# Kernel optimization log

Hardware: AMD Instinct MI355X
Metric: run time of the kernel (lower is better)

## Reference

```python
import jax, jax.numpy as jnp
import numpy as np

DIM, DEPTH, HEADS, DIM_HEAD, MLP_DIM = 512, 6, 8, 64, 2048
INNER = HEADS * DIM_HEAD
EPS = 1e-5


def _layernorm(x, s, b):
    mu = jnp.mean(x, axis=-1, keepdims=True)
    var = jnp.mean(jnp.square(x - mu), axis=-1, keepdims=True)
    return (x - mu) * jax.lax.rsqrt(var + EPS) * s + b


def setup_inputs() -> dict:
    key = jax.random.key(0)
    ks = jax.random.split(key, 12)
    d = {
        "x": jax.random.normal(ks[0], (8, 1024, DIM), dtype=jnp.float32),
        "ln1_s": jnp.ones((DEPTH, DIM), jnp.float32),
        "ln1_b": jnp.zeros((DEPTH, DIM), jnp.float32),
        "w_qkv": jax.random.normal(ks[1], (DEPTH, DIM, 3 * INNER), dtype=jnp.float32) * (DIM ** -0.5),
        "w_out": jax.random.normal(ks[2], (DEPTH, INNER, DIM), dtype=jnp.float32) * (INNER ** -0.5),
        "b_out": jnp.zeros((DEPTH, DIM), jnp.float32),
        "ln2_s": jnp.ones((DEPTH, DIM), jnp.float32),
        "ln2_b": jnp.zeros((DEPTH, DIM), jnp.float32),
        "w1": jax.random.normal(ks[3], (DEPTH, DIM, MLP_DIM), dtype=jnp.float32) * (DIM ** -0.5),
        "b1": jnp.zeros((DEPTH, MLP_DIM), jnp.float32),
        "w2": jax.random.normal(ks[4], (DEPTH, MLP_DIM, DIM), dtype=jnp.float32) * (MLP_DIM ** -0.5),
        "b2": jnp.zeros((DEPTH, DIM), jnp.float32),
    }
    return d


def reference(x, ln1_s, ln1_b, w_qkv, w_out, b_out, ln2_s, ln2_b, w1, b1, w2, b2):
    b, n, _ = x.shape
    scale = DIM_HEAD ** -0.5
    for i in range(DEPTH):
        # --- PreNorm Attention with residual ---
        h = _layernorm(x, ln1_s[i], ln1_b[i])
        qkv = h @ w_qkv[i]                                  # [b, n, 3*inner]
        q, k, v = jnp.split(qkv, 3, axis=-1)
        q = q.reshape(b, n, HEADS, DIM_HEAD)
        k = k.reshape(b, n, HEADS, DIM_HEAD)
        v = v.reshape(b, n, HEADS, DIM_HEAD)
        dots = jnp.einsum('bihd,bjhd->bhij', q, k) * scale  # [b, h, n, n]
        attn = jax.nn.softmax(dots, axis=-1)
        out = jnp.einsum('bhij,bjhd->bihd', attn, v).reshape(b, n, INNER)
        x = out @ w_out[i] + b_out[i] + x
        # --- PreNorm FeedForward with residual ---
        h = _layernorm(x, ln2_s[i], ln2_b[i])
        h = jax.nn.gelu(h @ w1[i] + b1[i], approximate=False)
        x = h @ w2[i] + b2[i] + x
    return x
```

## Files before the change

kernel.cpp:

```cpp
#include <hip/hip_runtime.h>
#include <cstdint>
#include <cstddef>

#define M_TOK 8192
#define DIMM  512
#define HEADS 8
#define DH    64
#define MLPD  2048
#define DEPTH 6

typedef unsigned short u16;
typedef unsigned int   u32;
typedef __attribute__((ext_vector_type(8))) short short8;
typedef __attribute__((ext_vector_type(4))) float f32x4;

__device__ __forceinline__ float bf2f(u16 u){ return __uint_as_float(((u32)u) << 16); }
__device__ __forceinline__ u16 f2bf(float f){
    u32 x = __float_as_uint(f);
    u32 r = x + 0x7fffu + ((x >> 16) & 1u);
    return (u16)(r >> 16);
}

__global__ void k_transpose_cvt(const float* __restrict__ in, u16* __restrict__ out, int R, int C){
    __shared__ u16 tile[32][33];
    size_t zoff = (size_t)blockIdx.z * R * C;
    in += zoff; out += zoff;
    int c0 = blockIdx.x * 32, r0 = blockIdx.y * 32;
    int tx = threadIdx.x, ty = threadIdx.y;
    #pragma unroll
    for (int i = 0; i < 32; i += 8)
        tile[ty + i][tx] = f2bf(in[(size_t)(r0 + ty + i) * C + c0 + tx]);
    __syncthreads();
    #pragma unroll
    for (int i = 0; i < 32; i += 8)
        out[(size_t)(c0 + ty + i) * R + r0 + tx] = tile[tx][ty + i];
}

__global__ __launch_bounds__(64) void k_layernorm(const float* __restrict__ x,
                                                  const float* __restrict__ s,
                                                  const float* __restrict__ b,
                                                  u16* __restrict__ out){
    int row = blockIdx.x;
    int lane = threadIdx.x;
    const float* xp = x + (size_t)row * DIMM + lane * 8;
    float v[8];
    #pragma unroll
    for (int c = 0; c < 8; c++) v[c] = xp[c];
    float sum = 0.f, sq = 0.f;
    #pragma unroll
    for (int c = 0; c < 8; c++){ sum += v[c]; sq += v[c] * v[c]; }
    #pragma unroll
    for (int m = 32; m >= 1; m >>= 1){
        sum += __shfl_xor(sum, m);
        sq  += __shfl_xor(sq,  m);
    }
    float mu  = sum * (1.f / DIMM);
    float var = sq * (1.f / DIMM) - mu * mu;
    float rs  = rsqrtf(var + 1e-5f);
    u16* op = out + (size_t)row * DIMM + lane * 8;
    #pragma unroll
    for (int c = 0; c < 8; c++){
        int col = lane * 8 + c;
        op[c] = f2bf((v[c] - mu) * rs * s[col] + b[col]);
    }
}

__device__ __forceinline__ float gelu_exact(float v){
    return 0.5f * v * (1.f + erff(v * 0.70710678118654752f));
}

#define LDT64 72

template<int MODE>
__global__ __launch_bounds__(256) void k_gemm128b(const u16* __restrict__ A,
                                                  const u16* __restrict__ Bt,
                                                  const float* __restrict__ bias,
                                                  u16* __restrict__ Cout,
                                                  int M, int N, int K){
    __shared__ u16 As[128 * LDT64];
    __shared__ u16 Bs[128 * LDT64];
    int m0 = blockIdx.y * 128, n0 = blockIdx.x * 128;
    int t = threadIdx.x;
    int w = t >> 6, lane = t & 63;
    int mi = lane & 15, quad = lane >> 4;
    int wr = w >> 1, wc = w & 1;
    int srow = t >> 1, scol = (t & 1) * 32;

    const u16* ag = A  + (size_t)(m0 + srow) * K + scol;
    const u16* bg = Bt + (size_t)(n0 + srow) * K + scol;

    f32x4 acc[4][4];
    #pragma unroll
    for (int mt = 0; mt < 4; mt++)
        #pragma unroll
        for (int nt = 0; nt < 4; nt++) acc[mt][nt] = (f32x4){0.f, 0.f, 0.f, 0.f};

    for (int k0 = 0; k0 < K; k0 += 64){
        uint4 a0 = *(const uint4*)(ag + k0);
        uint4 a1 = *(const uint4*)(ag + k0 + 8);
        uint4 a2 = *(const uint4*)(ag + k0 + 16);
        uint4 a3 = *(const uint4*)(ag + k0 + 24);
        uint4 b0 = *(const uint4*)(bg + k0);
        uint4 b1 = *(const uint4*)(bg + k0 + 8);
        uint4 b2 = *(const uint4*)(bg + k0 + 16);
        uint4 b3 = *(const uint4*)(bg + k0 + 24);
        __syncthreads();
        *(uint4*)&As[srow * LDT64 + scol]      = a0;
        *(uint4*)&As[srow * LDT64 + scol + 8]  = a1;
        *(uint4*)&As[srow * LDT64 + scol + 16] = a2;
        *(uint4*)&As[srow * LDT64 + scol + 24] = a3;
        *(uint4*)&Bs[srow * LDT64 + scol]      = b0;
        *(uint4*)&Bs[srow * LDT64 + scol + 8]  = b1;
        *(uint4*)&Bs[srow * LDT64 + scol + 16] = b2;
        *(uint4*)&Bs[srow * LDT64 + scol + 24] = b3;
        __syncthreads();
        #pragma unroll
        for (int kk = 0; kk < 64; kk += 32){
            short8 af[4], bf[4];
            #pragma unroll
            for (int mt = 0; mt < 4; mt++)
                af[mt] = *(const short8*)&As[(wr * 64 + mt * 16 + mi) * LDT64 + kk + quad * 8];
            #pragma unroll
            for (int nt = 0; nt < 4; nt++)
                bf[nt] = *(const short8*)&Bs[(wc * 64 + nt * 16 + mi) * LDT64 + kk + quad * 8];
            #pragma unroll
            for (int mt = 0; mt < 4; mt++)
                #pragma unroll
                for (int nt = 0; nt < 4; nt++)
                    acc[mt][nt] = __builtin_amdgcn_mfma_f32_16x16x32_bf16(af[mt], bf[nt], acc[mt][nt], 0, 0, 0);
        }
    }

    float bv[4];
    if (MODE == 1){
        #pragma unroll
        for (int nt = 0; nt < 4; nt++) bv[nt] = bias[n0 + wc * 64 + nt * 16 + mi];
    }
    __syncthreads();
    u16* cs = &As[w * 16 * LDT64];
    int erow = lane >> 2, ecol = (lane & 3) * 16;
    #pragma unroll
    for (int mt = 0; mt < 4; mt++){
        #pragma unroll
        for (int nt = 0; nt < 4; nt++)
            #pragma unroll
            for (int r = 0; r < 4; r++){
                float v = acc[mt][nt][r];
                if (MODE == 1) v = gelu_exact(v + bv[nt]);
                cs[(quad * 4 + r) * LDT64 + nt * 16 + mi] = f2bf(v);
            }
        uint4 c0 = *(const uint4*)&cs[erow * LDT64 + ecol];
        uint4 c1 = *(const uint4*)&cs[erow * LDT64 + ecol + 8];
        u16* cp = Cout + (size_t)(m0 + wr * 64 + mt * 16 + erow) * N + n0 + wc * 64 + ecol;
        *(uint4*)cp       = c0;
        *(uint4*)(cp + 8) = c1;
    }
}

__global__ __launch_bounds__(256) void k_gemm64_res(const u16* __restrict__ A,
                                                    const u16* __restrict__ Bt,
                                                    const float* __restrict__ bias,
                                                    float* __restrict__ xres,
                                                    int M, int N, int K){
    __shared__ u16 As[64 * LDT64];
    __shared__ u16 Bs[64 * LDT64];
    int m0 = blockIdx.y * 64, n0 = blockIdx.x * 64;
    int t = threadIdx.x;
    int w = t >> 6, lane = t & 63;
    int mi = lane & 15, quad = lane >> 4;
    int srow = t >> 2, scol = (t & 3) * 16;

    const u16* ag = A  + (size_t)(m0 + srow) * K + scol;
    const u16* bg = Bt + (size_t)(n0 + srow) * K + scol;

    f32x4 acc[4];
    #pragma unroll
    for (int tt = 0; tt < 4; tt++) acc[tt] = (f32x4){0.f, 0.f, 0.f, 0.f};

    for (int k0 = 0; k0 < K; k0 += 64){
        uint4 a0 = *(const uint4*)(ag + k0);
        uint4 a1 = *(const uint4*)(ag + k0 + 8);
        uint4 b0 = *(const uint4*)(bg + k0);
        uint4 b1 = *(const uint4*)(bg + k0 + 8);
        __syncthreads();
        *(uint4*)&As[srow * LDT64 + scol]     = a0;
        *(uint4*)&As[srow * LDT64 + scol + 8] = a1;
        *(uint4*)&Bs[srow * LDT64 + scol]     = b0;
        *(uint4*)&Bs[srow * LDT64 + scol + 8] = b1;
        __syncthreads();
        short8 af0 = *(const short8*)&As[(w * 16 + mi) * LDT64 + quad * 8];
        short8 af1 = *(const short8*)&As[(w * 16 + mi) * LDT64 + quad * 8 + 32];
        #pragma unroll
        for (int tt = 0; tt < 4; tt++){
            short8 bf0 = *(const short8*)&Bs[(tt * 16 + mi) * LDT64 + quad * 8];
            short8 bf1 = *(const short8*)&Bs[(tt * 16 + mi) * LDT64 + quad * 8 + 32];
            acc[tt] = __builtin_amdgcn_mfma_f32_16x16x32_bf16(af0, bf0, acc[tt], 0, 0, 0);
            acc[tt] = __builtin_amdgcn_mfma_f32_16x16x32_bf16(af1, bf1, acc[tt], 0, 0, 0);
        }
    }

    float bv[4];
    #pragma unroll
    for (int tt = 0; tt < 4; tt++) bv[tt] = bias[n0 + tt * 16 + mi];
    __syncthreads();
    float* cs = (w < 2) ? ((float*)As + w * 16 * LDT64)
                        : ((float*)Bs + (w - 2) * 16 * LDT64);
    #pragma unroll
    for (int tt = 0; tt < 4; tt++)
        #pragma unroll
        for (int r = 0; r < 4; r++)
            cs[(quad * 4 + r) * LDT64 + tt * 16 + mi] = acc[tt][r] + bv[tt];
    int erow = lane >> 2, ecol = (lane & 3) * 16;
    float* xp = xres + (size_t)(m0 + w * 16 + erow) * N + n0 + ecol;
    #pragma unroll
    for (int j = 0; j < 4; j++){
        float4 cv = *(const float4*)&cs[erow * LDT64 + ecol + j * 4];
        float4 xv = *(const float4*)(xp + j * 4);
        xv.x += cv.x; xv.y += cv.y; xv.z += cv.z; xv.w += cv.w;
        *(float4*)(xp + j * 4) = xv;
    }
}

#define LDK 72
#define C1_LOG2E 0.18033688011112042f
#define C2_LOG2E 11.541560327111707f

__global__ __launch_bounds__(256) void k_flash(const u16* __restrict__ qkv, u16* __restrict__ out){
    __shared__ u16 Ks[64 * LDK];
    __shared__ u16 Vt[80 * LDK];
    __shared__ u16 Ps[4][32 * LDK];
    int qt = blockIdx.x, h = blockIdx.y, b = blockIdx.z;
    int t = threadIdx.x;
    int w = t >> 6, lane = t & 63;
    int mi = lane & 15, quad = lane >> 4;

    for (int i = t; i < 16 * 64; i += 256){
        int d = i >> 6, kk = i & 63;
        Vt[(64 + d) * LDK + kk] = 0x3F80;
    }

    const u16* base = qkv + ((size_t)b * 1024) * 1536;
    int hoff = h * 64;

    short8 qf[2][2];
    #pragma unroll
    for (int qh = 0; qh < 2; qh++){
        int qrow = qt * 128 + w * 32 + qh * 16 + mi;
        const u16* qp = base + (size_t)qrow * 1536 + hoff + quad * 8;
        qf[qh][0] = *(const short8*)(qp);
        qf[qh][1] = *(const short8*)(qp + 32);
    }

    f32x4 o[2][4];
    f32x4 lacc[2];
    #pragma unroll
    for (int qh = 0; qh < 2; qh++){
        #pragma unroll
        for (int nb = 0; nb < 4; nb++) o[qh][nb] = (f32x4){0.f, 0.f, 0.f, 0.f};
        lacc[qh] = (f32x4){0.f, 0.f, 0.f, 0.f};
    }

    int kkey = t >> 2, kseg = t & 3;
    const u16* kgp = base + (size_t)kkey * 1536 + 512 + hoff + kseg * 16;
    int vkey = lane, vdg = w;
    const u16* vgp = base + (size_t)vkey * 1536 + 1024 + hoff + vdg * 16;

    for (int kt = 0; kt < 16; kt++){
        size_t koff = (size_t)kt * 64 * 1536;
        uint4 kv0 = *(const uint4*)(kgp + koff);
        uint4 kv1 = *(const uint4*)(kgp + koff + 8);
        uint4 vv0 = *(const uint4*)(vgp + koff);
        uint4 vv1 = *(const uint4*)(vgp + koff + 8);
        __syncthreads();
        *(uint4*)&Ks[kkey * LDK + kseg * 16]     = kv0;
        *(uint4*)&Ks[kkey * LDK + kseg * 16 + 8] = kv1;
        u16 vtmp[16];
        *(uint4*)&vtmp[0] = vv0;
        *(uint4*)&vtmp[8] = vv1;
        #pragma unroll
        for (int i = 0; i < 16; i++)
            Vt[(vdg * 16 + i) * LDK + vkey] = vtmp[i];
        __syncthreads();

        short8 kb[4][2];
        #pragma unroll
        for (int nb = 0; nb < 4; nb++){
            kb[nb][0] = *(const short8*)&Ks[(nb * 16 + mi) * LDK + quad * 8];
            kb[nb][1] = *(const short8*)&Ks[(nb * 16 + mi) * LDK + quad * 8 + 32];
        }
        #pragma unroll
        for (int qh = 0; qh < 2; qh++){
            #pragma unroll
            for (int nb = 0; nb < 4; nb++){
                f32x4 z = (f32x4){0.f, 0.f, 0.f, 0.f};
                z = __builtin_amdgcn_mfma_f32_16x16x32_bf16(qf[qh][0], kb[nb][0], z, 0, 0, 0);
                z = __builtin_amdgcn_mfma_f32_16x16x32_bf16(qf[qh][1], kb[nb][1], z, 0, 0, 0);
                #pragma unroll
                for (int r = 0; r < 4; r++)
                    Ps[w][(qh * 16 + quad * 4 + r) * LDK + nb * 16 + mi] =
                        f2bf(exp2f(fmaf(z[r], C1_LOG2E, -C2_LOG2E)));
            }
        }
        short8 vb[4][2], lb[2];
        #pragma unroll
        for (int nb = 0; nb < 4; nb++){
            vb[nb][0] = *(const short8*)&Vt[(nb * 16 + mi) * LDK + quad * 8];
            vb[nb][1] = *(const short8*)&Vt[(nb * 16 + mi) * LDK + quad * 8 + 32];
        }
        lb[0] = *(const short8*)&Vt[(64 + mi) * LDK + quad * 8];
        lb[1] = *(const short8*)&Vt[(64 + mi) * LDK + quad * 8 + 32];
        #pragma unroll
        for (int qh = 0; qh < 2; qh++){
            const short8 a0 = *(const short8*)&Ps[w][(qh * 16 + mi) * LDK + quad * 8];
            const short8 a1 = *(const short8*)&Ps[w][(qh * 16 + mi) * LDK + quad * 8 + 32];
            #pragma unroll
            for (int nb = 0; nb < 4; nb++){
                o[qh][nb] = __builtin_amdgcn_mfma_f32_16x16x32_bf16(a0, vb[nb][0], o[qh][nb], 0, 0, 0);
                o[qh][nb] = __builtin_amdgcn_mfma_f32_16x16x32_bf16(a1, vb[nb][1], o[qh][nb], 0, 0, 0);
            }
            lacc[qh] = __builtin_amdgcn_mfma_f32_16x16x32_bf16(a0, lb[0], lacc[qh], 0, 0, 0);
            lacc[qh] = __builtin_amdgcn_mfma_f32_16x16x32_bf16(a1, lb[1], lacc[qh], 0, 0, 0);
        }
    }
    #pragma unroll
    for (int qh = 0; qh < 2; qh++){
        float invl[4];
        #pragma unroll
        for (int r = 0; r < 4; r++) invl[r] = 1.f / lacc[qh][r];
        u16* op = out + ((size_t)b * 1024 + qt * 128 + w * 32 + qh * 16) * 512 + hoff;
        #pragma unroll
        for (int nb = 0; nb < 4; nb++)
            #pragma unroll
            for (int r = 0; r < 4; r++)
                op[(quad * 4 + r) * 512 + nb * 16 + mi] = f2bf(o[qh][nb][r] * invl[r]);
    }
}

extern "C" void kernel_launch(void* const* d_in, const int* in_sizes, int n_in,
                              void* d_out, int out_size, void* d_ws, size_t ws_size,
                              hipStream_t stream){
    const float* x_in  = (const float*)d_in[0];
    const float* ln1_s = (const float*)d_in[1];
    const float* ln1_b = (const float*)d_in[2];
    const float* w_qkv = (const float*)d_in[3];
    const float* w_out = (const float*)d_in[4];
    const float* b_out = (const float*)d_in[5];
    const float* ln2_s = (const float*)d_in[6];
    const float* ln2_b = (const float*)d_in[7];
    const float* w1    = (const float*)d_in[8];
    const float* b1    = (const float*)d_in[9];
    const float* w2    = (const float*)d_in[10];
    const float* b2    = (const float*)d_in[11];
    float* out = (float*)d_out;

    char* ws = (char*)d_ws;
    float* x_f32 = (float*)ws;   ws += (size_t)M_TOK * DIMM * 4;
    u16* bufA    = (u16*)ws;     ws += (size_t)M_TOK * DIMM * 2;
    u16* bufB    = (u16*)ws;     ws += (size_t)M_TOK * MLPD * 2;
    u16* wbase   = (u16*)ws;
    size_t per_layer_w = (size_t)(1536 + 512 + 2048 + 2048) * 512;

    size_t used_big = (size_t)(ws - (char*)d_ws) + per_layer_w * 2 * DEPTH;
    bool big = (ws_size >= used_big);

    u16* ln_out   = bufA;
    u16* attn_out = bufA;
    u16* qkv      = bufB;
    u16* mlp_h    = bufB;

    size_t x_bytes = (size_t)M_TOK * DIMM * sizeof(float);
    hipMemcpyAsync(x_f32, x_in, x_bytes, hipMemcpyDeviceToDevice, stream);

    const size_t off_qkv = 0;
    const size_t off_out = (size_t)1536 * 512;
    const size_t off_w1  = off_out + (size_t)512 * 512;
    const size_t off_w2  = off_w1 + (size_t)2048 * 512;

    if (big){
        k_transpose_cvt<<<dim3(48, 16, 6), dim3(32, 8), 0, stream>>>(w_qkv, wbase + off_qkv * DEPTH, 512, 1536);
        k_transpose_cvt<<<dim3(16, 16, 6), dim3(32, 8), 0, stream>>>(w_out, wbase + off_out * DEPTH, 512, 512);
        k_transpose_cvt<<<dim3(64, 16, 6), dim3(32, 8), 0, stream>>>(w1,    wbase + off_w1  * DEPTH, 512, 2048);
        k_transpose_cvt<<<dim3(16, 64, 6), dim3(32, 8), 0, stream>>>(w2,    wbase + off_w2  * DEPTH, 2048, 512);
    }

    for (int i = 0; i < DEPTH; i++){
        u16 *wqkvT, *woutT, *w1T, *w2T;
        if (big){
            wqkvT = wbase + off_qkv * DEPTH + (size_t)i * 1536 * 512;
            woutT = wbase + off_out * DEPTH + (size_t)i * 512 * 512;
            w1T   = wbase + off_w1  * DEPTH + (size_t)i * 2048 * 512;
            w2T   = wbase + off_w2  * DEPTH + (size_t)i * 512 * 2048;
        } else {
            wqkvT = wbase + off_qkv; woutT = wbase + off_out;
            w1T   = wbase + off_w1;  w2T   = wbase + off_w2;
            k_transpose_cvt<<<dim3(48, 16), dim3(32, 8), 0, stream>>>(w_qkv + (size_t)i * 512 * 1536, wqkvT, 512, 1536);
            k_transpose_cvt<<<dim3(16, 16), dim3(32, 8), 0, stream>>>(w_out + (size_t)i * 512 * 512,  woutT, 512, 512);
            k_transpose_cvt<<<dim3(64, 16), dim3(32, 8), 0, stream>>>(w1    + (size_t)i * 512 * 2048, w1T,   512, 2048);
            k_transpose_cvt<<<dim3(16, 64), dim3(32, 8), 0, stream>>>(w2    + (size_t)i * 2048 * 512, w2T,   2048, 512);
        }

        k_layernorm<<<dim3(M_TOK), dim3(64), 0, stream>>>(x_f32, ln1_s + i * 512, ln1_b + i * 512, ln_out);
        k_gemm128b<0><<<dim3(12, 64), dim3(256), 0, stream>>>(ln_out, wqkvT, nullptr, qkv,
                                                              M_TOK, 1536, 512);
        k_flash<<<dim3(8, 8, 8), dim3(256), 0, stream>>>(qkv, attn_out);
        k_gemm64_res<<<dim3(8, 128), dim3(256), 0, stream>>>(attn_out, woutT, b_out + i * 512, x_f32,
                                                             M_TOK, 512, 512);
        k_layernorm<<<dim3(M_TOK), dim3(64), 0, stream>>>(x_f32, ln2_s + i * 512, ln2_b + i * 512, ln_out);
        k_gemm128b<1><<<dim3(16, 64), dim3(256), 0, stream>>>(ln_out, w1T, b1 + i * 2048, mlp_h,
                                                              M_TOK, 2048, 512);
        k_gemm64_res<<<dim3(8, 128), dim3(256), 0, stream>>>(mlp_h, w2T, b2 + i * 512, x_f32,
                                                             M_TOK, 512, 2048);
    }
    hipMemcpyAsync(out, x_f32, x_bytes, hipMemcpyDeviceToDevice, stream);
}
```

Before: 1.262 ms.

## Prefetch GEMM tiles into registers, swap grid order, truncate softmax bf16 conversion

Both GEMM kernels now load the next K-slab from global memory into registers before the current slab's MFMA work runs. The aim is to hide global load latency behind compute. All GEMM and flash launches swap grid axes so consecutive blocks walk along M (or along batch-head) instead of N, which changes L2 reuse of weight and activation tiles. The attention probability conversion to bf16 now truncates instead of rounding, which saves a few ALU ops per element at some cost in precision.

```diff
diff --git a/kernel.cpp b/kernel.cpp
--- a/kernel.cpp
+++ b/kernel.cpp
@@ -20,6 +20,7 @@
     u32 r = x + 0x7fffu + ((x >> 16) & 1u);
     return (u16)(r >> 16);
 }
+__device__ __forceinline__ u16 f2bf_t(float f){ return (u16)(__float_as_uint(f) >> 16); }
 
 __global__ void k_transpose_cvt(const float* __restrict__ in, u16* __restrict__ out, int R, int C){
     __shared__ u16 tile[32][33];
@@ -79,7 +80,7 @@
                                                   int M, int N, int K){
     __shared__ u16 As[128 * LDT64];
     __shared__ u16 Bs[128 * LDT64];
-    int m0 = blockIdx.y * 128, n0 = blockIdx.x * 128;
+    int m0 = blockIdx.x * 128, n0 = blockIdx.y * 128;
     int t = threadIdx.x;
     int w = t >> 6, lane = t & 63;
     int mi = lane & 15, quad = lane >> 4;
@@ -95,24 +96,26 @@
         #pragma unroll
         for (int nt = 0; nt < 4; nt++) acc[mt][nt] = (f32x4){0.f, 0.f, 0.f, 0.f};
 
+    uint4 pa[4], pb[4];
+    #pragma unroll
+    for (int j = 0; j < 4; j++){
+        pa[j] = *(const uint4*)(ag + j * 8);
+        pb[j] = *(const uint4*)(bg + j * 8);
+    }
+
     for (int k0 = 0; k0 < K; k0 += 64){
-        uint4 a0 = *(const uint4*)(ag + k0);
-        uint4 a1 = *(const uint4*)(ag + k0 + 8);
-        uint4 a2 = *(const uint4*)(ag + k0 + 16);
-        uint4 a3 = *(const uint4*)(ag + k0 + 24);
-        uint4 b0 = *(const uint4*)(bg + k0);
-        uint4 b1 = *(const uint4*)(bg + k0 + 8);
-        uint4 b2 = *(const uint4*)(bg + k0 + 16);
-        uint4 b3 = *(const uint4*)(bg + k0 + 24);
-        __syncthreads();
-        *(uint4*)&As[srow * LDT64 + scol]      = a0;
-        *(uint4*)&As[srow * LDT64 + scol + 8]  = a1;
-        *(uint4*)&As[srow * LDT64 + scol + 16] = a2;
-        *(uint4*)&As[srow * LDT64 + scol + 24] = a3;
-        *(uint4*)&Bs[srow * LDT64 + scol]      = b0;
-        *(uint4*)&Bs[srow * LDT64 + scol + 8]  = b1;
-        *(uint4*)&Bs[srow * LDT64 + scol + 16] = b2;
-        *(uint4*)&Bs[srow * LDT64 + scol + 24] = b3;
+        __syncthreads();
+        #pragma unroll
+        for (int j = 0; j < 4; j++){
+            *(uint4*)&As[srow * LDT64 + scol + j * 8] = pa[j];
+            *(uint4*)&Bs[srow * LDT64 + scol + j * 8] = pb[j];
+        }
+        int kn = (k0 + 64 < K) ? (k0 + 64) : 0;
+        #pragma unroll
+        for (int j = 0; j < 4; j++){
+            pa[j] = *(const uint4*)(ag + kn + j * 8);
+            pb[j] = *(const uint4*)(bg + kn + j * 8);
+        }
         __syncthreads();
         #pragma unroll
         for (int kk = 0; kk < 64; kk += 32){
@@ -164,7 +167,7 @@
                                                     int M, int N, int K){
     __shared__ u16 As[64 * LDT64];
     __shared__ u16 Bs[64 * LDT64];
-    int m0 = blockIdx.y * 64, n0 = blockIdx.x * 64;
+    int m0 = blockIdx.x * 64, n0 = blockIdx.y * 64;
     int t = threadIdx.x;
     int w = t >> 6, lane = t & 63;
     int mi = lane & 15, quad = lane >> 4;
@@ -177,16 +180,19 @@
     #pragma unroll
     for (int tt = 0; tt < 4; tt++) acc[tt] = (f32x4){0.f, 0.f, 0.f, 0.f};
 
+    uint4 pa[2], pb[2];
+    pa[0] = *(const uint4*)(ag);     pa[1] = *(const uint4*)(ag + 8);
+    pb[0] = *(const uint4*)(bg);     pb[1] = *(const uint4*)(bg + 8);
+
     for (int k0 = 0; k0 < K; k0 += 64){
-        uint4 a0 = *(const uint4*)(ag + k0);
-        uint4 a1 = *(const uint4*)(ag + k0 + 8);
-        uint4 b0 = *(const uint4*)(bg + k0);
-        uint4 b1 = *(const uint4*)(bg + k0 + 8);
-        __syncthreads();
-        *(uint4*)&As[srow * LDT64 + scol]     = a0;
-        *(uint4*)&As[srow * LDT64 + scol + 8] = a1;
-        *(uint4*)&Bs[srow * LDT64 + scol]     = b0;
-        *(uint4*)&Bs[srow * LDT64 + scol + 8] = b1;
+        __syncthreads();
+        *(uint4*)&As[srow * LDT64 + scol]     = pa[0];
+        *(uint4*)&As[srow * LDT64 + scol + 8] = pa[1];
+        *(uint4*)&Bs[srow * LDT64 + scol]     = pb[0];
+        *(uint4*)&Bs[srow * LDT64 + scol + 8] = pb[1];
+        int kn = (k0 + 64 < K) ? (k0 + 64) : 0;
+        pa[0] = *(const uint4*)(ag + kn);     pa[1] = *(const uint4*)(ag + kn + 8);
+        pb[0] = *(const uint4*)(bg + kn);     pb[1] = *(const uint4*)(bg + kn + 8);
         __syncthreads();
         short8 af0 = *(const short8*)&As[(w * 16 + mi) * LDT64 + quad * 8];
         short8 af1 = *(const short8*)&As[(w * 16 + mi) * LDT64 + quad * 8 + 32];
@@ -229,7 +235,8 @@
     __shared__ u16 Ks[64 * LDK];
     __shared__ u16 Vt[80 * LDK];
     __shared__ u16 Ps[4][32 * LDK];
-    int qt = blockIdx.x, h = blockIdx.y, b = blockIdx.z;
+    int bh = blockIdx.x, qt = blockIdx.y;
+    int b = bh >> 3, h = bh & 7;
     int t = threadIdx.x;
     int w = t >> 6, lane = t & 63;
     int mi = lane & 15, quad = lane >> 4;
@@ -298,7 +305,7 @@
                 #pragma unroll
                 for (int r = 0; r < 4; r++)
                     Ps[w][(qh * 16 + quad * 4 + r) * LDK + nb * 16 + mi] =
-                        f2bf(exp2f(fmaf(z[r], C1_LOG2E, -C2_LOG2E)));
+                        f2bf_t(exp2f(fmaf(z[r], C1_LOG2E, -C2_LOG2E)));
             }
         }
         short8 vb[4][2], lb[2];
@@ -400,15 +407,15 @@
         }
 
         k_layernorm<<<dim3(M_TOK), dim3(64), 0, stream>>>(x_f32, ln1_s + i * 512, ln1_b + i * 512, ln_out);
-        k_gemm128b<0><<<dim3(12, 64), dim3(256), 0, stream>>>(ln_out, wqkvT, nullptr, qkv,
+        k_gemm128b<0><<<dim3(64, 12), dim3(256), 0, stream>>>(ln_out, wqkvT, nullptr, qkv,
                                                               M_TOK, 1536, 512);
-        k_flash<<<dim3(8, 8, 8), dim3(256), 0, stream>>>(qkv, attn_out);
-        k_gemm64_res<<<dim3(8, 128), dim3(256), 0, stream>>>(attn_out, woutT, b_out + i * 512, x_f32,
+        k_flash<<<dim3(64, 8), dim3(256), 0, stream>>>(qkv, attn_out);
+        k_gemm64_res<<<dim3(128, 8), dim3(256), 0, stream>>>(attn_out, woutT, b_out + i * 512, x_f32,
                                                              M_TOK, 512, 512);
         k_layernorm<<<dim3(M_TOK), dim3(64), 0, stream>>>(x_f32, ln2_s + i * 512, ln2_b + i * 512, ln_out);
-        k_gemm128b<1><<<dim3(16, 64), dim3(256), 0, stream>>>(ln_out, w1T, b1 + i * 2048, mlp_h,
+        k_gemm128b<1><<<dim3(64, 16), dim3(256), 0, stream>>>(ln_out, w1T, b1 + i * 2048, mlp_h,
                                                               M_TOK, 2048, 512);
-        k_gemm64_res<<<dim3(8, 128), dim3(256), 0, stream>>>(mlp_h, w2T, b2 + i * 512, x_f32,
+        k_gemm64_res<<<dim3(128, 8), dim3(256), 0, stream>>>(mlp_h, w2T, b2 + i * 512, x_f32,
                                                              M_TOK, 512, 2048);
     }
     hipMemcpyAsync(out, x_f32, x_bytes, hipMemcpyDeviceToDevice, stream);
```

Measured after the change: 2.589 ms. +105.1%, slower.
